# Kernel optimization log

Hardware: AMD Instinct MI355X
Metric: run time of the kernel (lower is better)

The kernel has to match this reference:

```python
import jax, jax.numpy as jnp
import numpy as np

LN_EPS = 1e-5


def _gconv(src, dst, x, W, b, n_nodes):
    # DGL GraphConv, norm='both': D_out^{-1/2} A D_in^{-1/2} x W + b
    E = src.shape[0]
    ones = jnp.ones((E,), dtype=x.dtype)
    out_deg = jnp.clip(jax.ops.segment_sum(ones, src, num_segments=n_nodes), 1.0)
    in_deg = jnp.clip(jax.ops.segment_sum(ones, dst, num_segments=n_nodes), 1.0)
    x = x * jax.lax.rsqrt(out_deg)[:, None]
    agg = jax.ops.segment_sum(x[src], dst, num_segments=n_nodes)  # [N, d]
    agg = agg * jax.lax.rsqrt(in_deg)[:, None]
    return agg @ W + b


def _branch(src, dst, x, W1, b1, W2, b2, n_nodes):
    h = jax.nn.relu(_gconv(src, dst, x, W1, b1, n_nodes))  # dropout: eval mode = identity
    return _gconv(src, dst, h, W2, b2, n_nodes)


def _layer_norm(x, g, b):
    mu = jnp.mean(x, axis=-1, keepdims=True)
    var = jnp.mean(jnp.square(x - mu), axis=-1, keepdims=True)
    return (x - mu) * jax.lax.rsqrt(var + LN_EPS) * g + b


def setup_inputs() -> dict:
    key = jax.random.key(0)
    ks = jax.random.split(key, 16)
    N, E, H = 50000, 800000, 128
    Hh = H // 2
    s = lambda fan: 1.0 / np.sqrt(fan)
    u = lambda k, shape, fan: jax.random.uniform(k, shape, jnp.float32, -s(fan), s(fan))
    return {
        "features": jax.random.normal(ks[0], (N, H), jnp.float32),
        "src": jax.random.randint(ks[1], (E,), 0, N),
        "dst": jax.random.randint(ks[2], (E,), 0, N),
        "W1a": u(ks[3], (H, H), H), "b1a": jnp.zeros((H,), jnp.float32),
        "W2a": u(ks[4], (H, Hh), H), "b2a": jnp.zeros((Hh,), jnp.float32),
        "W1b": u(ks[5], (H, H), H), "b1b": jnp.zeros((H,), jnp.float32),
        "W2b": u(ks[6], (H, Hh), H), "b2b": jnp.zeros((Hh,), jnp.float32),
        "Wf1": u(ks[7], (H, H), H), "bf1": u(ks[8], (H,), H),
        "Wf2": u(ks[9], (H, H), H), "bf2": u(ks[10], (H,), H),
        "ln_g": jnp.ones((H,), jnp.float32), "ln_b": jnp.zeros((H,), jnp.float32),
        "n_nodes": N,
    }


def reference(features, src, dst, W1a, b1a, W2a, b2a, W1b, b1b, W2b, b2b,
              Wf1, bf1, Wf2, bf2, ln_g, ln_b, n_nodes):
    ha = _branch(src, dst, features, W1a, b1a, W2a, b2a, n_nodes)  # [N, H/2]
    hb = _branch(src, dst, features, W1b, b1b, W2b, b2b, n_nodes)  # [N, H/2]
    h = jnp.concatenate([ha, hb], axis=-1)  # [N, H]
    h = features + _layer_norm(h, ln_g, ln_b)
    ff = jax.nn.relu(h @ Wf1 + bf1) @ Wf2 + bf2  # dropout eval = identity
    return h + ff
```

## Files before the change

kernel.cpp:

```cpp
#include <hip/hip_runtime.h>

#define LN_EPS 1e-5f
#define NBLK 512
#define BSH  7
#define MAXB 512

typedef __attribute__((ext_vector_type(8))) short bf16x8;
typedef __attribute__((ext_vector_type(4))) float f32x4;

#define MFMA_B16(a, b, c) __builtin_amdgcn_mfma_f32_16x16x32_bf16((a), (b), (c), 0, 0, 0)

__device__ __forceinline__ float bflo(unsigned int u) {
  return __builtin_bit_cast(float, u << 16);
}
__device__ __forceinline__ float bfhi(unsigned int u) {
  return __builtin_bit_cast(float, u & 0xffff0000u);
}
__device__ __forceinline__ float bfs(unsigned short u) {
  return __builtin_bit_cast(float, (unsigned int)u << 16);
}
__device__ __forceinline__ unsigned short f2bf(float f) {
  unsigned int u = __builtin_bit_cast(unsigned int, f);
  u += 0x7fffu + ((u >> 16) & 1u);
  return (unsigned short)(u >> 16);
}
__device__ __forceinline__ float degrs(int d) { return rsqrtf((float)max(d, 1)); }

__global__ __launch_bounds__(256)
void bucket_hist(const int* __restrict__ src, const int* __restrict__ dst,
                 int* __restrict__ blk_cnt, int E, int nbk) {
  __shared__ int h[2 * MAXB];
  int b = blockIdx.x, t = threadIdx.x;
  for (int i = t; i < nbk; i += 256) { h[i] = 0; h[MAXB + i] = 0; }
  __syncthreads();
  int chunk = (E + NBLK - 1) / NBLK;
  int beg = b * chunk, end = min(E, beg + chunk);
  for (int i = beg + t; i < end; i += 256) {
    atomicAdd(&h[dst[i] >> BSH], 1);
    atomicAdd(&h[MAXB + (src[i] >> BSH)], 1);
  }
  __syncthreads();
  for (int i = t; i < nbk; i += 256) {
    blk_cnt[(size_t)i * NBLK + b] = h[i];
    blk_cnt[(size_t)(nbk + i) * NBLK + b] = h[MAXB + i];
  }
}

__global__ __launch_bounds__(256)
void scan_partial_g(const int* __restrict__ v, int* __restrict__ part, int L) {
  __shared__ int sd[256];
  int base = blockIdx.x * 1024;
  int t = threadIdx.x;
  int s = 0;
#pragma unroll
  for (int i = 0; i < 4; ++i) { int idx = base + t * 4 + i; if (idx < L) s += v[idx]; }
  sd[t] = s; __syncthreads();
  for (int o = 128; o > 0; o >>= 1) { if (t < o) sd[t] += sd[t + o]; __syncthreads(); }
  if (t == 0) part[blockIdx.x] = sd[0];
}

__global__ __launch_bounds__(256)
void scan_final_g(const int* __restrict__ v, const int* __restrict__ part,
                  int* __restrict__ off, int L) {
  __shared__ int sd[256];
  __shared__ int pex_s;
  int base = blockIdx.x * 1024;
  int t = threadIdx.x;
  if (t < 64) {
    int p = 0;
    for (int i = t; i < (int)blockIdx.x; i += 64) p += part[i];
#pragma unroll
    for (int o = 1; o < 64; o <<= 1) p += __shfl_xor(p, o, 64);
    if (t == 0) pex_s = p;
  }
  int loc[4]; int s = 0;
#pragma unroll
  for (int i = 0; i < 4; ++i) {
    int idx = base + t * 4 + i;
    loc[i] = (idx < L) ? v[idx] : 0;
    s += loc[i];
  }
  sd[t] = s; __syncthreads();
  for (int o = 1; o < 256; o <<= 1) {
    int x = (t >= o) ? sd[t - o] : 0;
    __syncthreads();
    sd[t] += x;
    __syncthreads();
  }
  int excl = sd[t] - s + pex_s;
#pragma unroll
  for (int i = 0; i < 4; ++i) {
    int idx = base + t * 4 + i;
    if (idx < L) off[idx] = excl;
    excl += loc[i];
  }
}

__global__ __launch_bounds__(256)
void bucket_scatter(const int* __restrict__ src, const int* __restrict__ dst,
                    const int* __restrict__ off, unsigned int* __restrict__ pairs,
                    int E, int nbk) {
  __shared__ int cur[2 * MAXB];
  int b = blockIdx.x, t = threadIdx.x;
  for (int i = t; i < nbk; i += 256) {
    cur[i] = off[(size_t)i * NBLK + b];
    cur[MAXB + i] = off[(size_t)(nbk + i) * NBLK + b];
  }
  __syncthreads();
  int chunk = (E + NBLK - 1) / NBLK;
  int beg = b * chunk, end = min(E, beg + chunk);
  for (int i = beg + t; i < end; i += 256) {
    int d = dst[i], s = src[i];
    int p1 = atomicAdd(&cur[d >> BSH], 1);
    pairs[p1] = ((unsigned int)s << BSH) | (unsigned int)(d & 127);
    int p2 = atomicAdd(&cur[MAXB + (s >> BSH)], 1);
    pairs[p2] = (unsigned int)(s & 127);
  }
}

__global__ __launch_bounds__(256)
void bucket_deg_rowoff(const unsigned int* __restrict__ pairs, const int* __restrict__ off,
                       int* __restrict__ deg_d, int* __restrict__ deg_s,
                       int* __restrict__ row_off, int N, int E, int nbk) {
  __shared__ int h[128];
  int g = blockIdx.x, t = threadIdx.x;
  if (t < 128) h[t] = 0;
  __syncthreads();
  if (g < nbk) {
    int base = off[(size_t)g * NBLK];
    int end  = off[(size_t)(g + 1) * NBLK];
    for (int i = base + t; i < end; i += 256) atomicAdd(&h[pairs[i] & 127], 1);
    __syncthreads();
    int orig = (t < 128) ? h[t] : 0;
    for (int o = 1; o < 128; o <<= 1) {
      int v = (t < 128 && t >= o) ? h[t - o] : 0;
      __syncthreads();
      if (t < 128) h[t] += v;
      __syncthreads();
    }
    if (t < 128) {
      int node = (g << BSH) + t;
      if (node < N) {
        row_off[node] = base + h[t] - orig;
        deg_d[node] = orig;
      }
    }
    if (g == nbk - 1 && t == 0) row_off[N] = E;
  } else {
    int j = g - nbk;
    int beg = off[(size_t)(nbk + j) * NBLK];
    int end = (j + 1 < nbk) ? off[(size_t)(nbk + j + 1) * NBLK] : 2 * E;
    for (int i = beg + t; i < end; i += 256) atomicAdd(&h[pairs[i] & 127], 1);
    __syncthreads();
    int nb0 = j << BSH;
    if (t < 128 && nb0 + t < N) deg_s[nb0 + t] = h[t];
  }
}

__global__ __launch_bounds__(256)
void fill2_convert(const unsigned int* __restrict__ pairs, const int* __restrict__ off,
                   const int* __restrict__ row_off, int* __restrict__ csr_src,
                   int N, int E, int nbk,
                   const float* __restrict__ x, const int* __restrict__ deg_s,
                   unsigned short* __restrict__ xb, int n4,
                   const float* __restrict__ W1a, const float* __restrict__ W1b,
                   const float* __restrict__ W2a, const float* __restrict__ W2b,
                   const float* __restrict__ Wf1, const float* __restrict__ Wf2,
                   unsigned short* __restrict__ w1aT, unsigned short* __restrict__ w1bT,
                   unsigned short* __restrict__ w2aT, unsigned short* __restrict__ w2bT,
                   unsigned short* __restrict__ wf1T, unsigned short* __restrict__ wf2T) {
  const int featB = (n4 + 255) >> 8;
  int b = blockIdx.x, t = threadIdx.x;
  if (b < nbk) {
    __shared__ int cur[128];
    if (t < 128) {
      int node = (b << BSH) + t;
      cur[t] = (node < N) ? row_off[node] : 0;
    }
    __syncthreads();
    int beg = off[(size_t)b * NBLK];
    int end = off[(size_t)(b + 1) * NBLK];
    for (int i = beg + t; i < end; i += 256) {
      unsigned int v = pairs[i];
      int pos = atomicAdd(&cur[v & 127], 1);
      csr_src[pos] = (int)(v >> BSH);
    }
  } else if (b < nbk + featB) {
    int i = (b - nbk) * 256 + t;
    if (i < n4) {
      float sc = degrs(deg_s[i >> 5]);
      float4 v = reinterpret_cast<const float4*>(x)[i];
      ushort4 r;
      r.x = f2bf(v.x * sc); r.y = f2bf(v.y * sc); r.z = f2bf(v.z * sc); r.w = f2bf(v.w * sc);
      reinterpret_cast<ushort4*>(xb)[i] = r;
    }
  } else {
    const float* S; unsigned short* D; int NC;
    switch (b - nbk - featB) {
      case 0: S = W1a; D = w1aT; NC = 128; break;
      case 1: S = W1b; D = w1bT; NC = 128; break;
      case 2: S = W2a; D = w2aT; NC = 64;  break;
      case 3: S = W2b; D = w2bT; NC = 64;  break;
      case 4: S = Wf1; D = wf1T; NC = 128; break;
      default: S = Wf2; D = wf2T; NC = 128; break;
    }
    int total = 128 * NC;
    for (int i = t; i < total; i += 256) {
      int k = i / NC, n = i - k * NC;
      D[n * 128 + k] = f2bf(S[i]);
    }
  }
}

__global__ __launch_bounds__(256)
void gather128b(const int* __restrict__ row_off, const int* __restrict__ csr_src,
                const unsigned short* __restrict__ xb,
                unsigned short* __restrict__ ob, int N) {
  int n = blockIdx.x * 4 + (threadIdx.x >> 6);
  if (n >= N) return;
  int lane = threadIdx.x & 63;
  int ch = lane & 15, es = lane >> 4;
  int beg = row_off[n], end = row_off[n + 1];
  float a[8] = {0.f, 0.f, 0.f, 0.f, 0.f, 0.f, 0.f, 0.f};
  int k = beg + es;
  for (; k + 4 < end; k += 8) {
    int s0 = csr_src[k], s1 = csr_src[k + 4];
    uint4 v0 = *reinterpret_cast<const uint4*>(xb + (size_t)s0 * 128 + ch * 8);
    uint4 v1 = *reinterpret_cast<const uint4*>(xb + (size_t)s1 * 128 + ch * 8);
    a[0] += bflo(v0.x) + bflo(v1.x); a[1] += bfhi(v0.x) + bfhi(v1.x);
    a[2] += bflo(v0.y) + bflo(v1.y); a[3] += bfhi(v0.y) + bfhi(v1.y);
    a[4] += bflo(v0.z) + bflo(v1.z); a[5] += bfhi(v0.z) + bfhi(v1.z);
    a[6] += bflo(v0.w) + bflo(v1.w); a[7] += bfhi(v0.w) + bfhi(v1.w);
  }
  if (k < end) {
    int s0 = csr_src[k];
    uint4 v0 = *reinterpret_cast<const uint4*>(xb + (size_t)s0 * 128 + ch * 8);
    a[0] += bflo(v0.x); a[1] += bfhi(v0.x);
    a[2] += bflo(v0.y); a[3] += bfhi(v0.y);
    a[4] += bflo(v0.z); a[5] += bfhi(v0.z);
    a[6] += bflo(v0.w); a[7] += bfhi(v0.w);
  }
#pragma unroll
  for (int o = 16; o < 64; o <<= 1)
#pragma unroll
    for (int i = 0; i < 8; ++i) a[i] += __shfl_xor(a[i], o, 64);
  if (es == 0) {
    uint4 r;
    r.x = (unsigned int)f2bf(a[0]) | ((unsigned int)f2bf(a[1]) << 16);
    r.y = (unsigned int)f2bf(a[2]) | ((unsigned int)f2bf(a[3]) << 16);
    r.z = (unsigned int)f2bf(a[4]) | ((unsigned int)f2bf(a[5]) << 16);
    r.w = (unsigned int)f2bf(a[6]) | ((unsigned int)f2bf(a[7]) << 16);
    *reinterpret_cast<uint4*>(ob + (size_t)n * 128 + ch * 8) = r;
  }
}

__global__ __launch_bounds__(256, 6)
void gemm_mid_br(const unsigned short* __restrict__ aggb,
                 const unsigned short* __restrict__ w1aT, const float* __restrict__ b1a,
                 const unsigned short* __restrict__ w1bT, const float* __restrict__ b1b,
                 const unsigned short* __restrict__ w2aT,
                 const unsigned short* __restrict__ w2bT,
                 const int* __restrict__ deg_s, const int* __restrict__ deg_d,
                 unsigned short* __restrict__ zb, int N) {
  __shared__ unsigned short h1s[64 * 128];
  int br = blockIdx.y;
  const unsigned short* w1T = br ? w1bT : w1aT;
  const float* b1 = br ? b1b : b1a;
  const unsigned short* w2T = br ? w2bT : w2aT;
  int t = threadIdx.x, wid = t >> 6, lane = t & 63;
  int m0 = blockIdx.x * 64;
  int ll = lane & 15, lg = lane >> 4;
  int rA = wid * 16 + ll;
  int rw0 = m0 + wid * 16 + lg * 4;
  int rl0 = wid * 16 + lg * 4;

  const unsigned short* ap = aggb + (size_t)min(m0 + rA, N - 1) * 128 + lg * 8;
  bf16x8 A[4];
#pragma unroll
  for (int k = 0; k < 4; ++k) A[k] = *reinterpret_cast<const bf16x8*>(ap + k * 32);

  float rsi[4], rso[4];
#pragma unroll
  for (int j = 0; j < 4; ++j) {
    int m = min(rw0 + j, N - 1);
    rsi[j] = degrs(deg_d[m]);
    rso[j] = degrs(deg_s[m]);
  }

#pragma unroll
  for (int c = 0; c < 8; ++c) {
    const unsigned short* bp = w1T + (size_t)(c * 16 + ll) * 128 + lg * 8;
    f32x4 acc = {0.f, 0.f, 0.f, 0.f};
#pragma unroll
    for (int k = 0; k < 4; ++k)
      acc = MFMA_B16(A[k], *reinterpret_cast<const bf16x8*>(bp + k * 32), acc);
    int n = c * 16 + ll;
    float bv = b1[n];
#pragma unroll
    for (int j = 0; j < 4; ++j) {
      float v = fmaxf(fmaf(acc[j], rsi[j], bv), 0.f) * rso[j];
      int r = rl0 + j;
      h1s[r * 128 + (n ^ ((r & 7) << 3))] = f2bf(v);
    }
  }

  bf16x8 A2[4];
#pragma unroll
  for (int k = 0; k < 4; ++k)
    A2[k] = *reinterpret_cast<const bf16x8*>(
        h1s + rA * 128 + ((lg * 8 + k * 32) ^ ((rA & 7) << 3)));
#pragma unroll
  for (int c = 0; c < 4; ++c) {
    const unsigned short* bp = w2T + (size_t)(c * 16 + ll) * 128 + lg * 8;
    f32x4 acc = {0.f, 0.f, 0.f, 0.f};
#pragma unroll
    for (int k = 0; k < 4; ++k)
      acc = MFMA_B16(A2[k], *reinterpret_cast<const bf16x8*>(bp + k * 32), acc);
    int n = br * 64 + c * 16 + ll;
#pragma unroll
    for (int j = 0; j < 4; ++j) {
      int m = rw0 + j;
      if (m < N) zb[(size_t)m * 128 + n] = f2bf(acc[j]);
    }
  }
}

__global__ __launch_bounds__(128)
void fused_tail4(const unsigned short* __restrict__ agg2z,
                 const float* __restrict__ b2a, const float* __restrict__ b2b,
                 const float* __restrict__ feat, const int* __restrict__ deg_d,
                 const float* __restrict__ ln_g, const float* __restrict__ ln_b,
                 const unsigned short* __restrict__ wf1T, const float* __restrict__ bf1,
                 const unsigned short* __restrict__ wf2T, const float* __restrict__ bf2,
                 float* __restrict__ out, int N) {
  __shared__ unsigned short hsb[32 * 128];
  __shared__ unsigned short ffb[32 * 128];
  int t = threadIdx.x, wid = t >> 6, lane = t & 63;
  int m0 = blockIdx.x * 32;
  int ll = lane & 15, lg = lane >> 4;
  int rl0 = wid * 16 + lg * 4;

  float rsv[4];
#pragma unroll
  for (int j = 0; j < 4; ++j) rsv[j] = degrs(deg_d[min(m0 + rl0 + j, N - 1)]);

  float x[8][4];
  float s[4] = {0.f, 0.f, 0.f, 0.f}, q[4] = {0.f, 0.f, 0.f, 0.f};
#pragma unroll
  for (int ct = 0; ct < 8; ++ct) {
    int n = ct * 16 + ll;
    float bv = (n < 64) ? b2a[n] : b2b[n - 64];
#pragma unroll
    for (int j = 0; j < 4; ++j) {
      int m = min(m0 + rl0 + j, N - 1);
      float v = fmaf(bfs(agg2z[(size_t)m * 128 + n]), rsv[j], bv);
      x[ct][j] = v;
      s[j] += v;
      q[j] += v * v;
    }
  }

#pragma unroll
  for (int o = 1; o < 16; o <<= 1) {
#pragma unroll
    for (int j = 0; j < 4; ++j) {
      s[j] += __shfl_xor(s[j], o, 64);
      q[j] += __shfl_xor(q[j], o, 64);
    }
  }
  float mu[4], rstd[4];
#pragma unroll
  for (int j = 0; j < 4; ++j) {
    mu[j] = s[j] * (1.f / 128.f);
    float var = fmaxf(q[j] * (1.f / 128.f) - mu[j] * mu[j], 0.f);
    rstd[j] = rsqrtf(var + LN_EPS);
  }
#pragma unroll
  for (int ct = 0; ct < 8; ++ct) {
    int n = ct * 16 + ll;
    float gv = ln_g[n], bv = ln_b[n];
#pragma unroll
    for (int j = 0; j < 4; ++j) {
      int m = min(m0 + rl0 + j, N - 1);
      float hv = feat[(size_t)m * 128 + n] + (x[ct][j] - mu[j]) * rstd[j] * gv + bv;
      x[ct][j] = hv;
      int r = rl0 + j;
      hsb[r * 128 + (n ^ ((r & 7) << 3))] = f2bf(hv);
    }
  }

  {
    int rloc = wid * 16 + ll;
    int swr = (rloc & 7) << 3;
    bf16x8 A[4];
#pragma unroll
    for (int k = 0; k < 4; ++k)
      A[k] = *reinterpret_cast<const bf16x8*>(hsb + rloc * 128 + ((lg * 8 + k * 32) ^ swr));
#pragma unroll
    for (int c = 0; c < 8; ++c) {
      const unsigned short* bp = wf1T + (size_t)(c * 16 + ll) * 128 + lg * 8;
      f32x4 a = {0.f, 0.f, 0.f, 0.f};
#pragma unroll
      for (int k = 0; k < 4; ++k)
        a = MFMA_B16(A[k], *reinterpret_cast<const bf16x8*>(bp + k * 32), a);
      int n = c * 16 + ll;
      float bv = bf1[n];
#pragma unroll
      for (int j = 0; j < 4; ++j) {
        int r = rl0 + j;
        ffb[r * 128 + (n ^ ((r & 7) << 3))] = f2bf(fmaxf(a[j] + bv, 0.f));
      }
    }
  }

  {
    int rloc = wid * 16 + ll;
    int swr = (rloc & 7) << 3;
    bf16x8 A[4];
#pragma unroll
    for (int k = 0; k < 4; ++k)
      A[k] = *reinterpret_cast<const bf16x8*>(ffb + rloc * 128 + ((lg * 8 + k * 32) ^ swr));
#pragma unroll
    for (int c = 0; c < 8; ++c) {
      const unsigned short* bp = wf2T + (size_t)(c * 16 + ll) * 128 + lg * 8;
      f32x4 a = {0.f, 0.f, 0.f, 0.f};
#pragma unroll
      for (int k = 0; k < 4; ++k)
        a = MFMA_B16(A[k], *reinterpret_cast<const bf16x8*>(bp + k * 32), a);
      int n = c * 16 + ll;
      float bv = bf2[n];
#pragma unroll
      for (int j = 0; j < 4; ++j) {
        int m = m0 + rl0 + j;
        if (m < N) out[(size_t)m * 128 + n] = x[c][j] + a[j] + bv;
      }
    }
  }
}

extern "C" void kernel_launch(void* const* d_in, const int* in_sizes, int n_in,
                              void* d_out, int out_size, void* d_ws, size_t ws_size,
                              hipStream_t stream) {
  const float* features = (const float*)d_in[0];
  const int*   src      = (const int*)d_in[1];
  const int*   dst      = (const int*)d_in[2];
  const float* W1a = (const float*)d_in[3];  const float* b1a = (const float*)d_in[4];
  const float* W2a = (const float*)d_in[5];  const float* b2a = (const float*)d_in[6];
  const float* W1b = (const float*)d_in[7];  const float* b1b = (const float*)d_in[8];
  const float* W2b = (const float*)d_in[9];  const float* b2b = (const float*)d_in[10];
  const float* Wf1 = (const float*)d_in[11]; const float* bf1 = (const float*)d_in[12];
  const float* Wf2 = (const float*)d_in[13]; const float* bf2 = (const float*)d_in[14];
  const float* ln_g = (const float*)d_in[15];
  const float* ln_b = (const float*)d_in[16];

  const int N = in_sizes[0] / 128;
  const int E = in_sizes[1];
  float* out = (float*)d_out;

  const int nbk = (N + 127) >> BSH;
  const int L = 2 * nbk * NBLK;

  size_t off_b = 0;
  char* wsb = (char*)d_ws;
  auto take = [&](size_t bytes) -> void* {
    void* p = wsb + off_b;
    off_b += (bytes + 255) & ~(size_t)255;
    return p;
  };
  int* blk_cnt = (int*)take((size_t)L * 4);
  int* boff    = (int*)take((size_t)L * 4);
  int* part    = (int*)take((size_t)1024 * 4);
  unsigned int* pairs = (unsigned int*)take((size_t)2 * E * 4);
  int* deg_s   = (int*)take((size_t)N * 4);
  int* deg_d   = (int*)take((size_t)N * 4);
  int* row_off = (int*)take((size_t)(N + 1) * 4);
  int* csr_src = (int*)take((size_t)E * 4);
  unsigned short* featb = (unsigned short*)take((size_t)N * 128 * 2);
  unsigned short* aggb  = (unsigned short*)take((size_t)N * 128 * 2);
  unsigned short* zb    = (unsigned short*)take((size_t)N * 128 * 2);
  unsigned short* agg2z = (unsigned short*)take((size_t)N * 128 * 2);
  unsigned short* w1aT  = (unsigned short*)take(128 * 128 * 2);
  unsigned short* w1bT  = (unsigned short*)take(128 * 128 * 2);
  unsigned short* w2aT  = (unsigned short*)take(64 * 128 * 2);
  unsigned short* w2bT  = (unsigned short*)take(64 * 128 * 2);
  unsigned short* wf1T  = (unsigned short*)take(128 * 128 * 2);
  unsigned short* wf2T  = (unsigned short*)take(128 * 128 * 2);

  const int gatherBlocks = (N + 3) / 4;
  const int mtiles = (N + 63) / 64;
  const int ttiles = (N + 31) / 32;
  const int n4 = (N * 128) / 4;
  const int featB = (n4 + 255) / 256;
  const int scanL = (L + 1023) / 1024;

  bucket_hist<<<NBLK, 256, 0, stream>>>(src, dst, blk_cnt, E, nbk);
  scan_partial_g<<<scanL, 256, 0, stream>>>(blk_cnt, part, L);
  scan_final_g<<<scanL, 256, 0, stream>>>(blk_cnt, part, boff, L);
  bucket_scatter<<<NBLK, 256, 0, stream>>>(src, dst, boff, pairs, E, nbk);
  bucket_deg_rowoff<<<2 * nbk, 256, 0, stream>>>(pairs, boff, deg_d, deg_s,
                                                 row_off, N, E, nbk);
  fill2_convert<<<nbk + featB + 6, 256, 0, stream>>>(
      pairs, boff, row_off, csr_src, N, E, nbk,
      features, deg_s, featb, n4,
      W1a, W1b, W2a, W2b, Wf1, Wf2,
      w1aT, w1bT, w2aT, w2bT, wf1T, wf2T);
  gather128b<<<gatherBlocks, 256, 0, stream>>>(row_off, csr_src, featb, aggb, N);
  gemm_mid_br<<<dim3(mtiles, 2), 256, 0, stream>>>(aggb, w1aT, b1a, w1bT, b1b,
                                                   w2aT, w2bT, deg_s, deg_d, zb, N);
  gather128b<<<gatherBlocks, 256, 0, stream>>>(row_off, csr_src, zb, agg2z, N);
  fused_tail4<<<ttiles, 128, 0, stream>>>(agg2z, b2a, b2b,
                                          features, deg_d, ln_g, ln_b,
                                          wf1T, bf1, wf2T, bf2, out, N);
}
```

Measured before the change: 216.6 us.

## Fuse CSR fill into bucket pass and read bf16 features in tail

The CSR column fill moves into the degree/row-offset kernel, so each bucket scans its pairs once more from the same block and the row_off round trip through global memory goes away. The feature/weight conversion becomes its own kernel. The residual in the tail now reads the scaled bf16 feature copy and undoes the degree scaling with sqrt(deg_s), which halves residual read traffic but adds bf16 rounding error to the residual. The occupancy hint on gemm_mid_br is also removed.

New measurement: 217.5 us. No clear change (+0.4%).

```diff
diff --git a/kernel.cpp b/kernel.cpp
--- a/kernel.cpp
+++ b/kernel.cpp
@@ -119,10 +119,12 @@
 }
 
 __global__ __launch_bounds__(256)
-void bucket_deg_rowoff(const unsigned int* __restrict__ pairs, const int* __restrict__ off,
-                       int* __restrict__ deg_d, int* __restrict__ deg_s,
-                       int* __restrict__ row_off, int N, int E, int nbk) {
+void bucket_finish(const unsigned int* __restrict__ pairs, const int* __restrict__ off,
+                   int* __restrict__ row_off, int* __restrict__ deg_d,
+                   int* __restrict__ deg_s, int* __restrict__ csr_src,
+                   int N, int E, int nbk) {
   __shared__ int h[128];
+  __shared__ int cur[128];
   int g = blockIdx.x, t = threadIdx.x;
   if (t < 128) h[t] = 0;
   __syncthreads();
@@ -139,13 +141,18 @@
       __syncthreads();
     }
     if (t < 128) {
+      int excl = base + h[t] - orig;
+      cur[t] = excl;
       int node = (g << BSH) + t;
-      if (node < N) {
-        row_off[node] = base + h[t] - orig;
-        deg_d[node] = orig;
-      }
+      if (node < N) { row_off[node] = excl; deg_d[node] = orig; }
     }
     if (g == nbk - 1 && t == 0) row_off[N] = E;
+    __syncthreads();
+    for (int i = base + t; i < end; i += 256) {
+      unsigned int v = pairs[i];
+      int pos = atomicAdd(&cur[v & 127], 1);
+      csr_src[pos] = (int)(v >> BSH);
+    }
   } else {
     int j = g - nbk;
     int beg = off[(size_t)(nbk + j) * NBLK];
@@ -158,35 +165,18 @@
 }
 
 __global__ __launch_bounds__(256)
-void fill2_convert(const unsigned int* __restrict__ pairs, const int* __restrict__ off,
-                   const int* __restrict__ row_off, int* __restrict__ csr_src,
-                   int N, int E, int nbk,
-                   const float* __restrict__ x, const int* __restrict__ deg_s,
-                   unsigned short* __restrict__ xb, int n4,
-                   const float* __restrict__ W1a, const float* __restrict__ W1b,
-                   const float* __restrict__ W2a, const float* __restrict__ W2b,
-                   const float* __restrict__ Wf1, const float* __restrict__ Wf2,
-                   unsigned short* __restrict__ w1aT, unsigned short* __restrict__ w1bT,
-                   unsigned short* __restrict__ w2aT, unsigned short* __restrict__ w2bT,
-                   unsigned short* __restrict__ wf1T, unsigned short* __restrict__ wf2T) {
+void convert_all(const float* __restrict__ x, const int* __restrict__ deg_s,
+                 unsigned short* __restrict__ xb, int n4,
+                 const float* __restrict__ W1a, const float* __restrict__ W1b,
+                 const float* __restrict__ W2a, const float* __restrict__ W2b,
+                 const float* __restrict__ Wf1, const float* __restrict__ Wf2,
+                 unsigned short* __restrict__ w1aT, unsigned short* __restrict__ w1bT,
+                 unsigned short* __restrict__ w2aT, unsigned short* __restrict__ w2bT,
+                 unsigned short* __restrict__ wf1T, unsigned short* __restrict__ wf2T) {
   const int featB = (n4 + 255) >> 8;
   int b = blockIdx.x, t = threadIdx.x;
-  if (b < nbk) {
-    __shared__ int cur[128];
-    if (t < 128) {
-      int node = (b << BSH) + t;
-      cur[t] = (node < N) ? row_off[node] : 0;
-    }
-    __syncthreads();
-    int beg = off[(size_t)b * NBLK];
-    int end = off[(size_t)(b + 1) * NBLK];
-    for (int i = beg + t; i < end; i += 256) {
-      unsigned int v = pairs[i];
-      int pos = atomicAdd(&cur[v & 127], 1);
-      csr_src[pos] = (int)(v >> BSH);
-    }
-  } else if (b < nbk + featB) {
-    int i = (b - nbk) * 256 + t;
+  if (b < featB) {
+    int i = b * 256 + t;
     if (i < n4) {
       float sc = degrs(deg_s[i >> 5]);
       float4 v = reinterpret_cast<const float4*>(x)[i];
@@ -196,7 +186,7 @@
     }
   } else {
     const float* S; unsigned short* D; int NC;
-    switch (b - nbk - featB) {
+    switch (b - featB) {
       case 0: S = W1a; D = w1aT; NC = 128; break;
       case 1: S = W1b; D = w1bT; NC = 128; break;
       case 2: S = W2a; D = w2aT; NC = 64;  break;
@@ -254,7 +244,7 @@
   }
 }
 
-__global__ __launch_bounds__(256, 6)
+__global__ __launch_bounds__(256)
 void gemm_mid_br(const unsigned short* __restrict__ aggb,
                  const unsigned short* __restrict__ w1aT, const float* __restrict__ b1a,
                  const unsigned short* __restrict__ w1bT, const float* __restrict__ b1b,
@@ -327,8 +317,9 @@
 
 __global__ __launch_bounds__(128)
 void fused_tail4(const unsigned short* __restrict__ agg2z,
+                 const unsigned short* __restrict__ featb,
                  const float* __restrict__ b2a, const float* __restrict__ b2b,
-                 const float* __restrict__ feat, const int* __restrict__ deg_d,
+                 const int* __restrict__ deg_s, const int* __restrict__ deg_d,
                  const float* __restrict__ ln_g, const float* __restrict__ ln_b,
                  const unsigned short* __restrict__ wf1T, const float* __restrict__ bf1,
                  const unsigned short* __restrict__ wf2T, const float* __restrict__ bf2,
@@ -340,9 +331,13 @@
   int ll = lane & 15, lg = lane >> 4;
   int rl0 = wid * 16 + lg * 4;
 
-  float rsv[4];
-#pragma unroll
-  for (int j = 0; j < 4; ++j) rsv[j] = degrs(deg_d[min(m0 + rl0 + j, N - 1)]);
+  float rsv[4], sqs[4];
+#pragma unroll
+  for (int j = 0; j < 4; ++j) {
+    int m = min(m0 + rl0 + j, N - 1);
+    rsv[j] = degrs(deg_d[m]);
+    sqs[j] = sqrtf((float)max(deg_s[m], 1));
+  }
 
   float x[8][4];
   float s[4] = {0.f, 0.f, 0.f, 0.f}, q[4] = {0.f, 0.f, 0.f, 0.f};
@@ -382,7 +377,8 @@
 #pragma unroll
     for (int j = 0; j < 4; ++j) {
       int m = min(m0 + rl0 + j, N - 1);
-      float hv = feat[(size_t)m * 128 + n] + (x[ct][j] - mu[j]) * rstd[j] * gv + bv;
+      float fv = bfs(featb[(size_t)m * 128 + n]) * sqs[j];
+      float hv = fv + (x[ct][j] - mu[j]) * rstd[j] * gv + bv;
       x[ct][j] = hv;
       int r = rl0 + j;
       hsb[r * 128 + (n ^ ((r & 7) << 3))] = f2bf(hv);
@@ -497,10 +493,9 @@
   scan_partial_g<<<scanL, 256, 0, stream>>>(blk_cnt, part, L);
   scan_final_g<<<scanL, 256, 0, stream>>>(blk_cnt, part, boff, L);
   bucket_scatter<<<NBLK, 256, 0, stream>>>(src, dst, boff, pairs, E, nbk);
-  bucket_deg_rowoff<<<2 * nbk, 256, 0, stream>>>(pairs, boff, deg_d, deg_s,
-                                                 row_off, N, E, nbk);
-  fill2_convert<<<nbk + featB + 6, 256, 0, stream>>>(
-      pairs, boff, row_off, csr_src, N, E, nbk,
+  bucket_finish<<<2 * nbk, 256, 0, stream>>>(
+      pairs, boff, row_off, deg_d, deg_s, csr_src, N, E, nbk);
+  convert_all<<<featB + 6, 256, 0, stream>>>(
       features, deg_s, featb, n4,
       W1a, W1b, W2a, W2b, Wf1, Wf2,
       w1aT, w1bT, w2aT, w2bT, wf1T, wf2T);
@@ -508,7 +503,7 @@
   gemm_mid_br<<<dim3(mtiles, 2), 256, 0, stream>>>(aggb, w1aT, b1a, w1bT, b1b,
                                                    w2aT, w2bT, deg_s, deg_d, zb, N);
   gather128b<<<gatherBlocks, 256, 0, stream>>>(row_off, csr_src, zb, agg2z, N);
-  fused_tail4<<<ttiles, 128, 0, stream>>>(agg2z, b2a, b2b,
-                                          features, deg_d, ln_g, ln_b,
+  fused_tail4<<<ttiles, 128, 0, stream>>>(agg2z, featb, b2a, b2b,
+                                          deg_s, deg_d, ln_g, ln_b,
                                           wf1T, bf1, wf2T, bf2, out, N);
 }
```
